# Kernel optimization log

Measured on AMD Instinct MI355X. Metric: run time of the kernel, lower is better.

## Reference

```python
import jax, jax.numpy as jnp
import numpy as np

H, HKV, D, W = 64, 8, 64, 128          # heads, kv heads, head_dim, sliding window
G = H // HKV                            # query heads per kv head
HID = 2880
THETA = 150000.0
SCALE = D ** -0.5
NEG = -1e30


def _rope(x, positions):
    # x: [B,S,h,D]; GPT-NeoX style rotate_half RoPE
    half = D // 2
    inv_freq = 1.0 / (THETA ** (jnp.arange(0, half, dtype=jnp.float32) / half))
    ang = positions.astype(jnp.float32)[:, None] * inv_freq          # [S, D/2]
    cos = jnp.cos(ang)[None, :, None, :]
    sin = jnp.sin(ang)[None, :, None, :]
    x1, x2 = x[..., :half], x[..., half:]
    return jnp.concatenate([x1 * cos - x2 * sin, x2 * cos + x1 * sin], axis=-1)


def setup_inputs() -> dict:
    key = jax.random.key(0)
    ks = jax.random.split(key, 6)
    B, S = 1, 2048
    return {
        "hidden_states": jax.random.normal(ks[0], (B, S, HID), jnp.float32),
        "positions": jnp.arange(S, dtype=jnp.int32),
        "w_qkv": jax.random.normal(ks[1], (HID, (H + 2 * HKV) * D), jnp.float32) * 0.02,
        "b_qkv": jax.random.normal(ks[2], ((H + 2 * HKV) * D,), jnp.float32) * 0.02,
        "w_o": jax.random.normal(ks[3], (H * D, HID), jnp.float32) * 0.02,
        "b_o": jax.random.normal(ks[4], (HID,), jnp.float32) * 0.02,
        "sinks": jax.random.normal(ks[5], (H,), jnp.float32),
    }


def reference(hidden_states, positions, w_qkv, b_qkv, w_o, b_o, sinks):
    B, S, _ = hidden_states.shape
    qkv = hidden_states @ w_qkv + b_qkv                               # [B,S,(H+2Hkv)*D]
    q, k, v = jnp.split(qkv, [H * D, H * D + HKV * D], axis=-1)
    Q = q.reshape(B, S, H, D)
    K = k.reshape(B, S, HKV, D)
    V = v.reshape(B, S, HKV, D)
    Q = _rope(Q, positions)
    K = _rope(K, positions)

    # banded (sliding-window) key/value gather: query i sees keys i-W+1..i
    offsets = jnp.arange(W) - (W - 1)                                 # [-(W-1)..0]
    kidx = jnp.arange(S)[:, None] + offsets                           # [S,W]
    valid = kidx >= 0
    kidx = jnp.maximum(kidx, 0)
    Kw = K[:, kidx]                                                    # [B,S,W,HKV,D]
    Vw = V[:, kidx]

    Qr = Q.reshape(B, S, HKV, G, D)                                    # GQA grouping
    scores = jnp.einsum('bskgd,bswkd->bskgw', Qr, Kw) * SCALE          # [B,S,HKV,G,W]
    scores = jnp.where(valid[None, :, None, None, :], scores, NEG)

    sink = sinks.reshape(HKV, G)[None, None]                           # [1,1,HKV,G]
    m = jnp.maximum(scores.max(axis=-1), sink)                         # [B,S,HKV,G]
    p = jnp.exp(scores - m[..., None])
    denom = p.sum(axis=-1) + jnp.exp(sink - m)                         # sink in normalizer
    out = jnp.einsum('bskgw,bswkd->bskgd', p, Vw) / denom[..., None]

    out = out.reshape(B, S, H * D)
    return out @ w_o + b_o
```

## Files before the change

### kernel.cpp

```cpp
#include <hip/hip_runtime.h>

typedef unsigned short u16;
typedef __bf16 bf16x8 __attribute__((ext_vector_type(8)));
typedef float f32x4 __attribute__((ext_vector_type(4)));
typedef unsigned short u16x8 __attribute__((ext_vector_type(8)));

#define QKV_N 5120
#define SEQ 2048
#define ATTN_K 4096
#define KPAD 2944
#define SCALE 0.125f
#define NEGINF -1e30f

__device__ __forceinline__ u16 f2bf(float f) {
  unsigned int u = __builtin_bit_cast(unsigned int, f);
  u = (u + 0x7FFFu + ((u >> 16) & 1u)) >> 16;
  return (u16)u;
}

#define MFMA16(a, b, c) __builtin_amdgcn_mfma_f32_16x16x32_bf16((a), (b), (c), 0, 0, 0)

__device__ __forceinline__ void gl_lds16(const u16* g, u16* l) {
  __builtin_amdgcn_global_load_lds(
      (const __attribute__((address_space(1))) unsigned int*)(const void*)g,
      (__attribute__((address_space(3))) unsigned int*)(void*)l, 16, 0, 0);
}

__device__ __forceinline__ bf16x8 lds_frag(const u16* mat, int row, int kh, int lg) {
  int off = row * 128 + ((kh * 64 + lg * 16) ^ ((row & 7) << 4));
  return *(const bf16x8*)((const char*)mat + off);
}

__global__ __launch_bounds__(256) void k_rope_table(const int* __restrict__ pos,
                                                    float2* __restrict__ tab) {
  int t = blockIdx.x * 256 + threadIdx.x;
  int s = t >> 5, i = t & 31;
  float freq = powf(150000.0f, -(float)i * (1.0f / 32.0f));
  float ang = (float)pos[s] * freq;
  float sv, cv;
  sincosf(ang, &sv, &cv);
  tab[t] = make_float2(cv, sv);
}

__global__ __launch_bounds__(256) void k_convert_pad(const float* __restrict__ in,
                                                     u16* __restrict__ out) {
  int i = blockIdx.x * 256 + threadIdx.x;
  int r = i / 736, c4 = i - r * 736;
  if (r >= 2048) return;
  ushort4 o = {0, 0, 0, 0};
  if (c4 < 720) {
    float4 v = *(const float4*)(in + (size_t)r * 2880 + c4 * 4);
    o.x = f2bf(v.x); o.y = f2bf(v.y); o.z = f2bf(v.z); o.w = f2bf(v.w);
  }
  ((ushort4*)out)[(size_t)r * 736 + c4] = o;
}

__global__ __launch_bounds__(256) void k_transpose(const float* __restrict__ in,
                                                   u16* __restrict__ out,
                                                   int Kin, int Kout, int Nd, int Npad) {
  __shared__ float tile[32][33];
  int n0 = blockIdx.x * 32, k0 = blockIdx.y * 32;
  int c = threadIdx.x & 31, r0 = threadIdx.x >> 5;
#pragma unroll
  for (int j = 0; j < 4; j++) {
    int r = r0 + j * 8;
    float v = 0.f;
    if (n0 + c < Nd && k0 + r < Kin) v = in[(size_t)(k0 + r) * Nd + n0 + c];
    tile[r][c] = v;
  }
  __syncthreads();
#pragma unroll
  for (int j = 0; j < 4; j++) {
    int rr = r0 + j * 8;
    int n = n0 + rr;
    if (n < Npad) out[(size_t)n * Kout + k0 + c] = f2bf(tile[c][rr]);
  }
}

__global__ __launch_bounds__(512, 1) void k_gemm1(const u16* __restrict__ Ag,
                                                  const u16* __restrict__ Bg,
                                                  const float* __restrict__ bias,
                                                  const float2* __restrict__ tab,
                                                  u16* __restrict__ C) {
  __shared__ u16 ldsbuf[2][32768];
  const int tid = threadIdx.x;
  const int lane = tid & 63, wave = tid >> 6;
  const int wm = wave >> 2, wn = wave & 3;
  const int lr = lane & 15, lg = lane >> 4;
  int bid = blockIdx.x;
  int sb = (bid & 7) * 20 + (bid >> 3);
  const int m0 = (sb / 20) * 256, n0 = (sb % 20) * 256;

  f32x4 acc[8][4] = {};

  const int srow = wave * 8 + (lane >> 3);
  const int sc = ((lane & 7) ^ (lane >> 3)) << 3;
  const u16* gA = Ag + (size_t)(m0 + srow) * KPAD + sc;
  const u16* gB = Bg + (size_t)(n0 + srow) * KPAD + sc;

#define G1_STAGE(kt, b)                                                          \
  {                                                                              \
    u16* Ab = &ldsbuf[b][0];                                                     \
    u16* Bb = &ldsbuf[b][16384];                                                 \
    _Pragma("unroll") for (int r = 0; r < 4; r++) {                              \
      gl_lds16(gA + (size_t)(r * 64) * KPAD + (kt), Ab + (r * 64 + wave * 8) * 64); \
      gl_lds16(gB + (size_t)(r * 64) * KPAD + (kt), Bb + (r * 64 + wave * 8) * 64); \
    }                                                                            \
  }

  G1_STAGE(0, 0)
  G1_STAGE(64, 1)
  asm volatile("s_waitcnt vmcnt(8)" ::: "memory");
  __builtin_amdgcn_s_barrier();

  for (int t = 0; t < 46; t++) {
    const int b = t & 1;
    const u16* La = &ldsbuf[b][0];
    const u16* Lb = &ldsbuf[b][16384];
    bf16x8 Bf[4][2];
#pragma unroll
    for (int nf = 0; nf < 4; nf++)
#pragma unroll
      for (int kh = 0; kh < 2; kh++)
        Bf[nf][kh] = lds_frag(Lb, wn * 64 + nf * 16 + lr, kh, lg);
#pragma unroll
    for (int q = 0; q < 4; q++) {
      bf16x8 Af[2][2];
#pragma unroll
      for (int mi = 0; mi < 2; mi++)
#pragma unroll
        for (int kh = 0; kh < 2; kh++)
          Af[mi][kh] = lds_frag(La, wm * 128 + (q * 2 + mi) * 16 + lr, kh, lg);
      __builtin_amdgcn_s_barrier();
      __builtin_amdgcn_s_setprio(1);
#pragma unroll
      for (int mi = 0; mi < 2; mi++)
#pragma unroll
        for (int nf = 0; nf < 4; nf++)
#pragma unroll
          for (int kh = 0; kh < 2; kh++)
            acc[q * 2 + mi][nf] = MFMA16(Af[mi][kh], Bf[nf][kh], acc[q * 2 + mi][nf]);
      __builtin_amdgcn_s_setprio(0);
      __builtin_amdgcn_s_barrier();
    }
    if (t <= 43) {
      G1_STAGE((t + 2) * 64, b)
      asm volatile("s_waitcnt vmcnt(8)" ::: "memory");
    } else {
      asm volatile("s_waitcnt vmcnt(0)" ::: "memory");
    }
    __builtin_amdgcn_s_barrier();
  }
#undef G1_STAGE

  const bool rope = (n0 < 4608);
  if (rope) {
#pragma unroll
    for (int mf = 0; mf < 8; mf++)
#pragma unroll
      for (int nf = 0; nf < 2; nf++) {
        int col1 = n0 + wn * 64 + nf * 16 + lr;
        int col2 = col1 + 32;
        float b1 = bias[col1], b2 = bias[col2];
#pragma unroll
        for (int rg = 0; rg < 4; rg++) {
          int row = m0 + wm * 128 + mf * 16 + lg * 4 + rg;
          float2 cs = tab[(size_t)row * 32 + nf * 16 + lr];
          float x1 = acc[mf][nf][rg] + b1;
          float x2 = acc[mf][nf + 2][rg] + b2;
          C[(size_t)row * QKV_N + col1] = f2bf(x1 * cs.x - x2 * cs.y);
          C[(size_t)row * QKV_N + col2] = f2bf(x2 * cs.x + x1 * cs.y);
        }
      }
  } else {
#pragma unroll
    for (int mf = 0; mf < 8; mf++)
#pragma unroll
      for (int nf = 0; nf < 4; nf++) {
        int col = n0 + wn * 64 + nf * 16 + lr;
        float bv = bias[col];
#pragma unroll
        for (int rg = 0; rg < 4; rg++) {
          int row = m0 + wm * 128 + mf * 16 + lg * 4 + rg;
          C[(size_t)row * QKV_N + col] = f2bf(acc[mf][nf][rg] + bv);
        }
      }
  }
}

__global__ __launch_bounds__(256, 2) void k_gemm2(const u16* __restrict__ Ag,
                                                  const u16* __restrict__ Bg,
                                                  const float* __restrict__ bias,
                                                  float* __restrict__ C) {
  __shared__ u16 ldsbuf[2][16384];
  const int tid = threadIdx.x;
  const int lane = tid & 63, wave = tid >> 6;
  const int wm = wave >> 1, wn = wave & 1;
  const int lr = lane & 15, lg = lane >> 4;
  int bid = blockIdx.x;
  int sb = (bid & 7) * 46 + (bid >> 3);
  const int m0 = (sb / 23) * 128, n0 = (sb % 23) * 128;

  f32x4 acc[4][4] = {};

  const int srow = wave * 8 + (lane >> 3);
  const int sc = ((lane & 7) ^ (lane >> 3)) << 3;
  const u16* gA = Ag + (size_t)(m0 + srow) * ATTN_K + sc;
  const u16* gB = Bg + (size_t)(n0 + srow) * ATTN_K + sc;

#define G2_STAGE(kt, b)                                                          \
  {                                                                              \
    u16* Ab = &ldsbuf[b][0];                                                     \
    u16* Bb = &ldsbuf[b][8192];                                                  \
    _Pragma("unroll") for (int r = 0; r < 4; r++) {                              \
      gl_lds16(gA + (size_t)(r * 32) * ATTN_K + (kt), Ab + (r * 32 + wave * 8) * 64); \
      gl_lds16(gB + (size_t)(r * 32) * ATTN_K + (kt), Bb + (r * 32 + wave * 8) * 64); \
    }                                                                            \
  }

  G2_STAGE(0, 0)
  G2_STAGE(64, 1)
  asm volatile("s_waitcnt vmcnt(8)" ::: "memory");
  __builtin_amdgcn_s_barrier();

  for (int t = 0; t < 64; t++) {
    const int b = t & 1;
    const u16* La = &ldsbuf[b][0];
    const u16* Lb = &ldsbuf[b][8192];
    bf16x8 Bf[4][2];
#pragma unroll
    for (int nf = 0; nf < 4; nf++)
#pragma unroll
      for (int kh = 0; kh < 2; kh++)
        Bf[nf][kh] = lds_frag(Lb, wn * 64 + nf * 16 + lr, kh, lg);
#pragma unroll
    for (int q = 0; q < 2; q++) {
      bf16x8 Af[2][2];
#pragma unroll
      for (int mi = 0; mi < 2; mi++)
#pragma unroll
        for (int kh = 0; kh < 2; kh++)
          Af[mi][kh] = lds_frag(La, wm * 64 + (q * 2 + mi) * 16 + lr, kh, lg);
      __builtin_amdgcn_s_barrier();
      __builtin_amdgcn_s_setprio(1);
#pragma unroll
      for (int mi = 0; mi < 2; mi++)
#pragma unroll
        for (int nf = 0; nf < 4; nf++)
#pragma unroll
          for (int kh = 0; kh < 2; kh++)
            acc[q * 2 + mi][nf] = MFMA16(Af[mi][kh], Bf[nf][kh], acc[q * 2 + mi][nf]);
      __builtin_amdgcn_s_setprio(0);
      __builtin_amdgcn_s_barrier();
    }
    if (t <= 61) {
      G2_STAGE((t + 2) * 64, b)
      asm volatile("s_waitcnt vmcnt(8)" ::: "memory");
    } else {
      asm volatile("s_waitcnt vmcnt(0)" ::: "memory");
    }
    __builtin_amdgcn_s_barrier();
  }
#undef G2_STAGE

#pragma unroll
  for (int mi = 0; mi < 4; mi++)
#pragma unroll
    for (int ni = 0; ni < 4; ni++) {
      int row = m0 + wm * 64 + mi * 16 + lg * 4;
      int col = n0 + wn * 64 + ni * 16 + lr;
      if (col < 2880) {
        float bv = bias[col];
#pragma unroll
        for (int rg = 0; rg < 4; rg++)
          C[(size_t)(row + rg) * 2880 + col] = acc[mi][ni][rg] + bv;
      }
    }
}

__global__ __launch_bounds__(512, 2) void k_attn(const u16* __restrict__ qkv,
                                                 const float* __restrict__ sinks,
                                                 u16* __restrict__ out) {
  __shared__ u16 Klds[160 * 64];
  __shared__ u16 Vt[64 * 168];
  __shared__ u16 Pslab[8 * 32 * 40];
  const int hk = blockIdx.y;
  const int s0 = blockIdx.x * 32;
  const int kb = s0 - 127;
  const int tid = threadIdx.x;
  const int lane = tid & 63, w = tid >> 6;
  const int lr = lane & 15, lg = lane >> 4;

  for (int ch = tid; ch < 160 * 8; ch += 512) {
    int key = ch >> 3, c = ch & 7;
    int kidx = kb + key;
    u16x8 val = {0, 0, 0, 0, 0, 0, 0, 0};
    if (kidx >= 0 && kidx < SEQ)
      val = *(const u16x8*)(qkv + (size_t)kidx * QKV_N + 4096 + hk * 64 + c * 8);
    int off = (key * 128 + c * 16) ^ ((key & 7) << 4);
    *(u16x8*)((char*)Klds + off) = val;
  }
  for (int e4 = tid; e4 < 160 * 16; e4 += 512) {
    int key = e4 >> 4, d0 = (e4 & 15) * 4;
    int kidx = kb + key;
    ushort4 v = {0, 0, 0, 0};
    if (kidx >= 0 && kidx < SEQ)
      v = *(const ushort4*)(qkv + (size_t)kidx * QKV_N + 4608 + hk * 64 + d0);
    Vt[(d0 + 0) * 168 + key] = v.x;
    Vt[(d0 + 1) * 168 + key] = v.y;
    Vt[(d0 + 2) * 168 + key] = v.z;
    Vt[(d0 + 3) * 168 + key] = v.w;
  }

  const int head = hk * 8 + w;
  bf16x8 qf[2][2];
#pragma unroll
  for (int rt = 0; rt < 2; rt++)
#pragma unroll
    for (int ks = 0; ks < 2; ks++)
      qf[rt][ks] = *(const bf16x8*)(qkv + (size_t)(s0 + rt * 16 + lr) * QKV_N +
                                    head * 64 + ks * 32 + lg * 8);
  __syncthreads();

  f32x4 sc[2][10];
  f32x4 zz = {0.f, 0.f, 0.f, 0.f};
#pragma unroll
  for (int rt = 0; rt < 2; rt++)
#pragma unroll
    for (int nt = 0; nt < 10; nt++) sc[rt][nt] = zz;
#pragma unroll
  for (int nt = 0; nt < 10; nt++) {
    int key = nt * 16 + lr;
#pragma unroll
    for (int ks = 0; ks < 2; ks++) {
      int off = (key * 128 + ks * 64 + lg * 16) ^ ((key & 7) << 4);
      bf16x8 kf = *(const bf16x8*)((const char*)Klds + off);
      sc[0][nt] = MFMA16(qf[0][ks], kf, sc[0][nt]);
      sc[1][nt] = MFMA16(qf[1][ks], kf, sc[1][nt]);
    }
  }

#pragma unroll
  for (int rt = 0; rt < 2; rt++)
#pragma unroll
    for (int nt = 0; nt < 10; nt++)
#pragma unroll
      for (int rg = 0; rg < 4; rg++) {
        int qq = rt * 16 + lg * 4 + rg;
        int j = nt * 16 + lr;
        bool valid = (j >= qq) && (j <= qq + 127) && ((kb + j) >= 0);
        sc[rt][nt][rg] = valid ? sc[rt][nt][rg] * SCALE : NEGINF;
      }

  const float sink = sinks[head];
  float den[2][4];
#pragma unroll
  for (int rt = 0; rt < 2; rt++)
#pragma unroll
    for (int rg = 0; rg < 4; rg++) {
      float m = NEGINF;
#pragma unroll
      for (int nt = 0; nt < 10; nt++) m = fmaxf(m, sc[rt][nt][rg]);
#pragma unroll
      for (int x = 1; x < 16; x <<= 1) m = fmaxf(m, __shfl_xor(m, x, 64));
      m = fmaxf(m, sink);
      float sum = 0.f;
#pragma unroll
      for (int nt = 0; nt < 10; nt++) {
        float p = __expf(sc[rt][nt][rg] - m);
        sc[rt][nt][rg] = p;
        sum += p;
      }
#pragma unroll
      for (int x = 1; x < 16; x <<= 1) sum += __shfl_xor(sum, x, 64);
      den[rt][rg] = sum + __expf(sink - m);
    }

  f32x4 oacc[2][4];
#pragma unroll
  for (int rt = 0; rt < 2; rt++)
#pragma unroll
    for (int dn = 0; dn < 4; dn++) oacc[rt][dn] = zz;
  u16* slab = &Pslab[w * 32 * 40];
#pragma unroll
  for (int kt = 0; kt < 5; kt++) {
#pragma unroll
    for (int rt = 0; rt < 2; rt++)
#pragma unroll
      for (int j2 = 0; j2 < 2; j2++)
#pragma unroll
        for (int rg = 0; rg < 4; rg++)
          slab[(rt * 16 + lg * 4 + rg) * 40 + j2 * 16 + lr] = f2bf(sc[rt][kt * 2 + j2][rg]);
    asm volatile("s_waitcnt lgkmcnt(0)" ::: "memory");
    __builtin_amdgcn_sched_barrier(0);
    bf16x8 pf0 = *(const bf16x8*)&slab[lr * 40 + lg * 8];
    bf16x8 pf1 = *(const bf16x8*)&slab[(16 + lr) * 40 + lg * 8];
#pragma unroll
    for (int dn = 0; dn < 4; dn++) {
      bf16x8 vf = *(const bf16x8*)&Vt[(dn * 16 + lr) * 168 + kt * 32 + lg * 8];
      oacc[0][dn] = MFMA16(pf0, vf, oacc[0][dn]);
      oacc[1][dn] = MFMA16(pf1, vf, oacc[1][dn]);
    }
  }

#pragma unroll
  for (int rt = 0; rt < 2; rt++)
#pragma unroll
    for (int dn = 0; dn < 4; dn++)
#pragma unroll
      for (int rg = 0; rg < 4; rg++) {
        int s = s0 + rt * 16 + lg * 4 + rg;
        float val = oacc[rt][dn][rg] / den[rt][rg];
        out[(size_t)s * ATTN_K + head * 64 + dn * 16 + lr] = f2bf(val);
      }
}

extern "C" void kernel_launch(void* const* d_in, const int* in_sizes, int n_in,
                              void* d_out, int out_size, void* d_ws, size_t ws_size,
                              hipStream_t stream) {
  const float* hs = (const float*)d_in[0];
  const int* pos = (const int*)d_in[1];
  const float* wqkv = (const float*)d_in[2];
  const float* bqkv = (const float*)d_in[3];
  const float* wo = (const float*)d_in[4];
  const float* bo = (const float*)d_in[5];
  const float* sinks = (const float*)d_in[6];
  float* out = (float*)d_out;

  char* ws = (char*)d_ws;
  u16* qkvb = (u16*)(ws + 0);
  u16* hsb = (u16*)(ws + 41943040);
  u16* wqkvT = (u16*)(ws + 54001664);
  u16* attnb = (u16*)(ws + 41943040);
  u16* woT = (u16*)(ws + 84148224);
  float2* tab = (float2*)(ws + 108265472);

  k_rope_table<<<256, 256, 0, stream>>>(pos, tab);
  k_convert_pad<<<5888, 256, 0, stream>>>(hs, hsb);
  k_transpose<<<dim3(160, 92), 256, 0, stream>>>(wqkv, wqkvT, 2880, KPAD, 5120, 5120);
  k_transpose<<<dim3(92, 128), 256, 0, stream>>>(wo, woT, 4096, 4096, 2880, 2944);
  k_gemm1<<<160, 512, 0, stream>>>(hsb, wqkvT, bqkv, tab, qkvb);
  k_attn<<<dim3(64, 8), 512, 0, stream>>>(qkvb, sinks, attnb);
  k_gemm2<<<368, 256, 0, stream>>>(attnb, woT, bo, out);
}
```

Measured before the change: 221.4 us.

## Restructure QKV GEMM into half-K phased pipeline and prefetch A fragments in output GEMM

The QKV projection GEMM now splits each 64-wide K tile into two 32-wide halves with their own LDS layout and swizzle. It interleaves the global-to-LDS staging of the next tile across eight compute phases, so memory loads overlap MFMA work at a finer grain. The output projection GEMM loads the next A fragments before the current MFMAs and drops the per-quarter barriers, keeping one barrier per K tile. This aims to cut barrier stalls and LDS latency exposure, at the cost of more complex scheduling, extra registers, and a new LDS layout whose correctness depends on matching swizzles.

```diff
diff --git a/kernel.cpp b/kernel.cpp
--- a/kernel.cpp
+++ b/kernel.cpp
@@ -24,6 +24,10 @@
   __builtin_amdgcn_global_load_lds(
       (const __attribute__((address_space(1))) unsigned int*)(const void*)g,
       (__attribute__((address_space(3))) unsigned int*)(void*)l, 16, 0, 0);
+}
+
+__device__ __forceinline__ bf16x8 fragrd(const u16* base, int row, int rb) {
+  return *(const bf16x8*)((const char*)(base + row * 32) + rb);
 }
 
 __device__ __forceinline__ bf16x8 lds_frag(const u16* mat, int row, int kh, int lg) {
@@ -82,7 +86,8 @@
                                                   const float* __restrict__ bias,
                                                   const float2* __restrict__ tab,
                                                   u16* __restrict__ C) {
-  __shared__ u16 ldsbuf[2][32768];
+  __shared__ u16 lds_[2][32768];
+  u16* L = &lds_[0][0];
   const int tid = threadIdx.x;
   const int lane = tid & 63, wave = tid >> 6;
   const int wm = wave >> 2, wn = wave & 3;
@@ -92,66 +97,80 @@
   const int m0 = (sb / 20) * 256, n0 = (sb % 20) * 256;
 
   f32x4 acc[8][4] = {};
-
-  const int srow = wave * 8 + (lane >> 3);
-  const int sc = ((lane & 7) ^ (lane >> 3)) << 3;
-  const u16* gA = Ag + (size_t)(m0 + srow) * KPAD + sc;
-  const u16* gB = Bg + (size_t)(n0 + srow) * KPAD + sc;
-
-#define G1_STAGE(kt, b)                                                          \
-  {                                                                              \
-    u16* Ab = &ldsbuf[b][0];                                                     \
-    u16* Bb = &ldsbuf[b][16384];                                                 \
-    _Pragma("unroll") for (int r = 0; r < 4; r++) {                              \
-      gl_lds16(gA + (size_t)(r * 64) * KPAD + (kt), Ab + (r * 64 + wave * 8) * 64); \
-      gl_lds16(gB + (size_t)(r * 64) * KPAD + (kt), Bb + (r * 64 + wave * 8) * 64); \
-    }                                                                            \
-  }
-
-  G1_STAGE(0, 0)
-  G1_STAGE(64, 1)
-  asm volatile("s_waitcnt vmcnt(8)" ::: "memory");
+  bf16x8 Bf[4];
+
+  const int srow = wave * 16 + (lane >> 2);
+  const int xsl = (((lane & 3) ^ ((lane >> 2) & 3)) << 3);
+  const int rb = (lg * 16) ^ ((lr & 3) << 4);
+
+#define G1_STAGE_A(b, kh, kt)                                                   \
+  { _Pragma("unroll") for (int r_ = 0; r_ < 2; r_++) {                          \
+      gl_lds16(Ag + (size_t)(m0 + r_ * 128 + srow) * KPAD + (kt) + (kh) * 32 + xsl, \
+               L + (b) * 32768 + (kh) * 8192 + (r_ * 128 + wave * 16) * 32); } }
+#define G1_STAGE_B(b, kh, kt)                                                   \
+  { _Pragma("unroll") for (int r_ = 0; r_ < 2; r_++) {                          \
+      gl_lds16(Bg + (size_t)(n0 + r_ * 128 + srow) * KPAD + (kt) + (kh) * 32 + xsl, \
+               L + (b) * 32768 + 16384 + (kh) * 8192 + (r_ * 128 + wave * 16) * 32); } }
+
+#define VM4 asm volatile("s_waitcnt vmcnt(4)" ::: "memory");
+#define VM0 asm volatile("s_waitcnt vmcnt(0)" ::: "memory");
+
+#define PHASE(bb, kh, mh, LOADB, STAGE_STMT, WAIT_STMT)                         \
+  {                                                                             \
+    if (LOADB) {                                                                \
+      _Pragma("unroll") for (int nf = 0; nf < 4; nf++)                          \
+        Bf[nf] = fragrd(L + (bb) * 32768 + 16384 + (kh) * 8192,                 \
+                        wn * 64 + nf * 16 + lr, rb);                            \
+    }                                                                           \
+    bf16x8 Af[4];                                                               \
+    _Pragma("unroll") for (int mi = 0; mi < 4; mi++)                            \
+      Af[mi] = fragrd(L + (bb) * 32768 + (kh) * 8192,                           \
+                      wm * 128 + ((mh) * 4 + mi) * 16 + lr, rb);                \
+    STAGE_STMT;                                                                 \
+    WAIT_STMT;                                                                  \
+    __builtin_amdgcn_s_barrier();                                               \
+    asm volatile("s_waitcnt lgkmcnt(0)" ::: "memory");                          \
+    __builtin_amdgcn_sched_barrier(0);                                          \
+    __builtin_amdgcn_s_setprio(1);                                              \
+    _Pragma("unroll") for (int mi = 0; mi < 4; mi++)                            \
+      _Pragma("unroll") for (int nf = 0; nf < 4; nf++)                          \
+        acc[(mh) * 4 + mi][nf] = MFMA16(Af[mi], Bf[nf], acc[(mh) * 4 + mi][nf]); \
+    __builtin_amdgcn_s_setprio(0);                                              \
+    __builtin_amdgcn_s_barrier();                                               \
+  }
+
+  G1_STAGE_A(0, 0, 0)
+  G1_STAGE_B(0, 0, 0)
+  G1_STAGE_A(0, 1, 0)
+  G1_STAGE_B(0, 1, 0)
+  VM4
   __builtin_amdgcn_s_barrier();
 
-  for (int t = 0; t < 46; t++) {
-    const int b = t & 1;
-    const u16* La = &ldsbuf[b][0];
-    const u16* Lb = &ldsbuf[b][16384];
-    bf16x8 Bf[4][2];
-#pragma unroll
-    for (int nf = 0; nf < 4; nf++)
-#pragma unroll
-      for (int kh = 0; kh < 2; kh++)
-        Bf[nf][kh] = lds_frag(Lb, wn * 64 + nf * 16 + lr, kh, lg);
-#pragma unroll
-    for (int q = 0; q < 4; q++) {
-      bf16x8 Af[2][2];
-#pragma unroll
-      for (int mi = 0; mi < 2; mi++)
-#pragma unroll
-        for (int kh = 0; kh < 2; kh++)
-          Af[mi][kh] = lds_frag(La, wm * 128 + (q * 2 + mi) * 16 + lr, kh, lg);
-      __builtin_amdgcn_s_barrier();
-      __builtin_amdgcn_s_setprio(1);
-#pragma unroll
-      for (int mi = 0; mi < 2; mi++)
-#pragma unroll
-        for (int nf = 0; nf < 4; nf++)
-#pragma unroll
-          for (int kh = 0; kh < 2; kh++)
-            acc[q * 2 + mi][nf] = MFMA16(Af[mi][kh], Bf[nf][kh], acc[q * 2 + mi][nf]);
-      __builtin_amdgcn_s_setprio(0);
-      __builtin_amdgcn_s_barrier();
-    }
-    if (t <= 43) {
-      G1_STAGE((t + 2) * 64, b)
-      asm volatile("s_waitcnt vmcnt(8)" ::: "memory");
-    } else {
-      asm volatile("s_waitcnt vmcnt(0)" ::: "memory");
-    }
-    __builtin_amdgcn_s_barrier();
-  }
-#undef G1_STAGE
+#define G1_ITER(ii, TAILV)                                                      \
+  {                                                                             \
+    const int ktB = (2 * (ii) + 1) * 64;                                        \
+    const int ktC = (2 * (ii) + 2) * 64;                                        \
+    PHASE(0, 0, 0, true,  { G1_STAGE_A(1, 0, ktB) }, {})                        \
+    PHASE(0, 0, 1, false, { G1_STAGE_B(1, 0, ktB) }, VM4)                       \
+    PHASE(0, 1, 0, true,  { G1_STAGE_A(1, 1, ktB) }, {})                        \
+    PHASE(0, 1, 1, false, { G1_STAGE_B(1, 1, ktB) }, VM4)                       \
+    PHASE(1, 0, 0, true,  { if (!(TAILV)) G1_STAGE_A(0, 0, ktC) }, {})          \
+    PHASE(1, 0, 1, false, { if (!(TAILV)) G1_STAGE_B(0, 0, ktC) },              \
+          { if (TAILV) { VM0 } else { VM4 } })                                  \
+    PHASE(1, 1, 0, true,  { if (!(TAILV)) G1_STAGE_A(0, 1, ktC) }, {})          \
+    PHASE(1, 1, 1, false, { if (!(TAILV)) G1_STAGE_B(0, 1, ktC) },              \
+          { if (!(TAILV)) { VM4 } })                                            \
+  }
+
+  for (int i = 0; i < 22; i++) {
+    G1_ITER(i, false)
+  }
+  G1_ITER(22, true)
+
+#undef G1_ITER
+#undef PHASE
+#undef G1_STAGE_A
+#undef G1_STAGE_B
 
   const bool rope = (n0 < 4608);
   if (rope) {
@@ -233,15 +252,22 @@
 #pragma unroll
       for (int kh = 0; kh < 2; kh++)
         Bf[nf][kh] = lds_frag(Lb, wn * 64 + nf * 16 + lr, kh, lg);
+    bf16x8 Af[2][2];
+#pragma unroll
+    for (int mi = 0; mi < 2; mi++)
+#pragma unroll
+      for (int kh = 0; kh < 2; kh++)
+        Af[mi][kh] = lds_frag(La, wm * 64 + mi * 16 + lr, kh, lg);
 #pragma unroll
     for (int q = 0; q < 2; q++) {
-      bf16x8 Af[2][2];
-#pragma unroll
-      for (int mi = 0; mi < 2; mi++)
-#pragma unroll
-        for (int kh = 0; kh < 2; kh++)
-          Af[mi][kh] = lds_frag(La, wm * 64 + (q * 2 + mi) * 16 + lr, kh, lg);
-      __builtin_amdgcn_s_barrier();
+      bf16x8 An[2][2];
+      if (q < 1) {
+#pragma unroll
+        for (int mi = 0; mi < 2; mi++)
+#pragma unroll
+          for (int kh = 0; kh < 2; kh++)
+            An[mi][kh] = lds_frag(La, wm * 64 + ((q + 1) * 2 + mi) * 16 + lr, kh, lg);
+      }
       __builtin_amdgcn_s_setprio(1);
 #pragma unroll
       for (int mi = 0; mi < 2; mi++)
@@ -251,8 +277,15 @@
           for (int kh = 0; kh < 2; kh++)
             acc[q * 2 + mi][nf] = MFMA16(Af[mi][kh], Bf[nf][kh], acc[q * 2 + mi][nf]);
       __builtin_amdgcn_s_setprio(0);
-      __builtin_amdgcn_s_barrier();
-    }
+      if (q < 1) {
+#pragma unroll
+        for (int mi = 0; mi < 2; mi++)
+#pragma unroll
+          for (int kh = 0; kh < 2; kh++)
+            Af[mi][kh] = An[mi][kh];
+      }
+    }
+    __builtin_amdgcn_s_barrier();
     if (t <= 61) {
       G2_STAGE((t + 2) * 64, b)
       asm volatile("s_waitcnt vmcnt(8)" ::: "memory");
```

New measurement: 210.3 us. 1.05x faster.
